# Optimization experiments

Measured on AMD Instinct MI355X. Metric: run time of the kernel, lower is better.

## Reference

```python
import jax, jax.numpy as jnp
import numpy as np


def _maxpool3d(x):
    # 3x3x3 max pool, stride 1, padding 1 (torch pads with -inf for max pool)
    return jax.lax.reduce_window(
        x, -jnp.inf, jax.lax.max,
        window_dimensions=(1, 1, 3, 3, 3),
        window_strides=(1, 1, 1, 1, 1),
        padding=[(0, 0), (0, 0), (1, 1), (1, 1), (1, 1)],
    )


def _soft_erode(x):
    return -_maxpool3d(-x)


def _soft_dilate(x):
    return _maxpool3d(x)


def _soft_open(x):
    return _soft_dilate(_soft_erode(x))


def setup_inputs() -> dict:
    key = jax.random.key(0)
    img = jax.random.uniform(key, (2, 1, 192, 256, 256), dtype=jnp.float32)
    return {"img": img}


def reference(img):
    # NOTE: in the original torch module, `skel` is computed via soft_close +
    # an iterative relu(skel - soft_open(skel)) loop, but the final line
    # `skel = F.relu(img - soft_open(img))` overwrites it entirely, so the
    # loop is dead code and the output depends only on img.
    opened = _soft_open(img)  # dilate(erode(img)), morphological opening
    return jax.nn.relu(img - opened)
```

## Files before the change

kernel.cpp:

```cpp
#include <hip/hip_runtime.h>
#include <math.h>


#define D_ 192
#define H_ 256
#define W_ 256
#define NB 2
#define TH 32
#define TW 64
#define CD 16
#define NCHUNK (D_ / CD)

#define RAW_H (TH + 4)
#define RAW_W (TW + 8)
#define RAW_S 76
#define EB_H  (TH + 2)
#define EB_W  (TW + 8)
#define EB_S  76

#define NRAWF4 (RAW_H * (RAW_W / 4))
#define NBTASK (EB_H * (EB_W / 8))

__device__ __forceinline__ float min3f(float a, float b, float c) {
    return fminf(fminf(a, b), c);
}
__device__ __forceinline__ float max3f(float a, float b, float c) {
    return fmaxf(fmaxf(a, b), c);
}

__global__ __launch_bounds__(256, 3)
void soft_skel_v6(const float* __restrict__ img, float* __restrict__ out) {
    __shared__ __align__(16) float raw[RAW_H][RAW_S];
    __shared__ __align__(16) float ebuf[EB_H][EB_S];

    const int tid  = threadIdx.x;
    const int lane = tid & 63;
    const int w0 = blockIdx.x * TW;
    const int h0 = blockIdx.y * TH;
    const int n  = blockIdx.z / NCHUNK;
    const int ch = blockIdx.z - n * NCHUNK;
    const int z0 = ch * CD;

    const float* vol  = img + (size_t)n * (D_ * H_ * W_);
    float*       ovol = out + (size_t)n * (D_ * H_ * W_);

    const float PINF = INFINITY;

    bool a_slot[3], a_img[3];
    int  a_lds[3], a_off[3];
    #pragma unroll
    for (int k = 0; k < 3; ++k) {
        int idx = tid + 256 * k;
        bool slot = idx < NRAWF4;
        int row = idx / (RAW_W / 4);
        int cg  = idx - row * (RAW_W / 4);
        int gh = h0 - 2 + row;
        int gw = w0 - 4 + 4 * cg;
        a_slot[k] = slot;
        a_img[k]  = slot && (gh >= 0) && (gh < H_) && (gw >= 0) && (gw <= W_ - 4);
        a_off[k]  = gh * W_ + gw;
        a_lds[k]  = slot ? (row * RAW_S + 4 * cg) : 0;
    }

    const int  r0 = tid / 9;
    const int  c0 = (tid - r0 * 9) * 8;
    const bool has1 = tid < (NBTASK - 256);
    const int  t1 = tid + 256;
    const int  r1 = t1 / 9;
    const int  c1 = (t1 - r1 * 9) * 8;

    const int ty = tid >> 3;
    const int cx = tid & 7;
    const int xx = cx * 8;

    float pm0[8], sp0[8], pm1[8], sp1[8];
    float t2A[8], t2B[8], t2C[8];
    float rwA[8], rwB[8], rwC[8];
    #pragma unroll
    for (int j = 0; j < 8; ++j) {
        pm0[j] = sp0[j] = pm1[j] = sp1[j] = PINF;
        t2A[j] = t2B[j] = 0.f;
        rwA[j] = rwB[j] = 0.f;
    }

    auto prefetch = [&](int zz, float4 L[3]) {
        const bool zok = (zz >= 0) && (zz < D_);
        const float* plane = vol + (size_t)zz * (H_ * W_);
        #pragma unroll
        for (int k = 0; k < 3; ++k) {
            float4 v = make_float4(PINF, PINF, PINF, PINF);
            if (zok && a_img[k]) v = *(const float4*)(plane + a_off[k]);
            L[k] = v;
        }
    };

    auto btask = [&](int r, int cb, float pm[8], float sp[8], bool zeok) {
        float4 q00 = *(const float4*)(&raw[r][cb]);
        float4 q01 = *(const float4*)(&raw[r][cb + 4]);
        float4 q10 = *(const float4*)(&raw[r + 1][cb]);
        float4 q11 = *(const float4*)(&raw[r + 1][cb + 4]);
        float4 q20 = *(const float4*)(&raw[r + 2][cb]);
        float4 q21 = *(const float4*)(&raw[r + 2][cb + 4]);
        float v[8];
        v[0] = min3f(q00.x, q10.x, q20.x);
        v[1] = min3f(q00.y, q10.y, q20.y);
        v[2] = min3f(q00.z, q10.z, q20.z);
        v[3] = min3f(q00.w, q10.w, q20.w);
        v[4] = min3f(q01.x, q11.x, q21.x);
        v[5] = min3f(q01.y, q11.y, q21.y);
        v[6] = min3f(q01.z, q11.z, q21.z);
        v[7] = min3f(q01.w, q11.w, q21.w);

        float vL = __shfl_up(v[7], 1);
        float vR = __shfl_down(v[0], 1);
        if (lane == 0) {
            int cl = cb - 1; if (cl < 0) cl = 0;
            vL = min3f(raw[r][cl], raw[r + 1][cl], raw[r + 2][cl]);
        }
        if (lane == 63) {
            int cr = cb + 8; if (cr > RAW_W - 1) cr = RAW_W - 1;
            vR = min3f(raw[r][cr], raw[r + 1][cr], raw[r + 2][cr]);
        }

        float s[8];
        s[0] = min3f(vL, v[0], v[1]);
        #pragma unroll
        for (int j = 1; j < 7; ++j) s[j] = min3f(v[j - 1], v[j], v[j + 1]);
        s[7] = min3f(v[6], v[7], vR);

        const bool rok = zeok && ((unsigned)(h0 - 1 + r) < (unsigned)H_);
        float e[8];
        #pragma unroll
        for (int j = 0; j < 8; ++j) {
            float ev = fminf(pm[j], s[j]);
            bool ok = rok && ((unsigned)(w0 - 4 + cb + j) < (unsigned)W_);
            e[j] = ok ? ev : -PINF;
            pm[j] = fminf(sp[j], s[j]);
            sp[j] = s[j];
        }
        *(float4*)&ebuf[r][cb]     = make_float4(e[0], e[1], e[2], e[3]);
        *(float4*)&ebuf[r][cb + 4] = make_float4(e[4], e[5], e[6], e[7]);
    };

    float4 L[3];
    prefetch(z0 - 2, L);
    const int zzend = z0 + CD + 1;

    for (int zz = z0 - 2; zz <= zzend; ++zz) {
        #pragma unroll
        for (int k = 0; k < 3; ++k)
            if (a_slot[k]) *(float4*)(&raw[0][0] + a_lds[k]) = L[k];
        if (zz < zzend) prefetch(zz + 1, L);
        __syncthreads();

        float4 c0v, c1v;
        const bool zcok = (zz >= 0) && (zz < D_);
        if (zcok) {
            const float* cp = vol + ((size_t)zz * H_ + (h0 + ty)) * W_ + (w0 + xx);
            c0v = *(const float4*)cp;
            c1v = *(const float4*)(cp + 4);
        } else {
            c0v = c1v = make_float4(0.f, 0.f, 0.f, 0.f);
        }

        const int  ze   = zz - 1;
        const bool zeok = (ze >= 0) && (ze < D_);
        btask(r0, c0, pm0, sp0, zeok);
        if (has1) btask(r1, c1, pm1, sp1, zeok);

        rwC[0] = c0v.x; rwC[1] = c0v.y; rwC[2] = c0v.z; rwC[3] = c0v.w;
        rwC[4] = c1v.x; rwC[5] = c1v.y; rwC[6] = c1v.z; rwC[7] = c1v.w;
        __syncthreads();

        {
            const float* p0 = &ebuf[ty][0];
            const float* p1 = &ebuf[ty + 1][0];
            const float* p2 = &ebuf[ty + 2][0];
            float4 q00 = *(const float4*)(p0 + xx + 4);
            float4 q01 = *(const float4*)(p0 + xx + 8);
            float4 q10 = *(const float4*)(p1 + xx + 4);
            float4 q11 = *(const float4*)(p1 + xx + 8);
            float4 q20 = *(const float4*)(p2 + xx + 4);
            float4 q21 = *(const float4*)(p2 + xx + 8);
            float t[8];
            t[0] = max3f(q00.x, q10.x, q20.x);
            t[1] = max3f(q00.y, q10.y, q20.y);
            t[2] = max3f(q00.z, q10.z, q20.z);
            t[3] = max3f(q00.w, q10.w, q20.w);
            t[4] = max3f(q01.x, q11.x, q21.x);
            t[5] = max3f(q01.y, q11.y, q21.y);
            t[6] = max3f(q01.z, q11.z, q21.z);
            t[7] = max3f(q01.w, q11.w, q21.w);

            float tL = __shfl_up(t[7], 1);
            float tR = __shfl_down(t[0], 1);
            if (cx == 0) {
                tL = max3f(p0[xx + 3], p1[xx + 3], p2[xx + 3]);
            }
            if (cx == 7) {
                tR = max3f(p0[xx + 12], p1[xx + 12], p2[xx + 12]);
            }
            t2C[0] = max3f(tL, t[0], t[1]);
            #pragma unroll
            for (int j = 1; j < 7; ++j) t2C[j] = max3f(t[j - 1], t[j], t[j + 1]);
            t2C[7] = max3f(t[6], t[7], tR);
        }

        if (zz >= z0 + 2) {
            const int z = zz - 2;
            float* op = ovol + ((size_t)z * H_ + (h0 + ty)) * W_ + (w0 + xx);
            float o[8];
            #pragma unroll
            for (int j = 0; j < 8; ++j) {
                float opened = max3f(t2A[j], t2B[j], t2C[j]);
                float v = rwA[j] - opened;
                o[j] = v > 0.f ? v : 0.f;
            }
            *(float4*)op       = make_float4(o[0], o[1], o[2], o[3]);
            *(float4*)(op + 4) = make_float4(o[4], o[5], o[6], o[7]);
        }

        #pragma unroll
        for (int j = 0; j < 8; ++j) {
            t2A[j] = t2B[j]; t2B[j] = t2C[j];
            rwA[j] = rwB[j]; rwB[j] = rwC[j];
        }
    }
}

extern "C" void kernel_launch(void* const* d_in, const int* in_sizes, int n_in,
                              void* d_out, int out_size, void* d_ws, size_t ws_size,
                              hipStream_t stream) {
    const float* img = (const float*)d_in[0];
    float* out = (float*)d_out;

    dim3 grid(W_ / TW, H_ / TH, NB * NCHUNK);
    dim3 block(256);
    soft_skel_v6<<<grid, block, 0, stream>>>(img, out);
}
```

Baseline: 195.7 us.

## Double-buffer raw and erosion LDS tiles to drop one barrier per plane

Double-buffers the raw-input and eroded-plane shared-memory tiles so the erosion of plane z and the dilation of plane z-1 run between a single barrier per iteration instead of two. The center voxel values are now read from the previous raw tile in LDS instead of being reloaded from global memory. This adds one more pipeline stage, so each chunk does one extra iteration, and doubles LDS use, which may lower occupancy.

```diff
diff --git a/kernel.cpp b/kernel.cpp
--- a/kernel.cpp
+++ b/kernel.cpp
@@ -29,9 +29,9 @@
 }
 
 __global__ __launch_bounds__(256, 3)
-void soft_skel_v6(const float* __restrict__ img, float* __restrict__ out) {
-    __shared__ __align__(16) float raw[RAW_H][RAW_S];
-    __shared__ __align__(16) float ebuf[EB_H][EB_S];
+void soft_skel_v7(const float* __restrict__ img, float* __restrict__ out) {
+    __shared__ __align__(16) float raw[2][RAW_H][RAW_S];
+    __shared__ __align__(16) float ebuf[2][EB_H][EB_S];
 
     const int tid  = threadIdx.x;
     const int lane = tid & 63;
@@ -75,12 +75,12 @@
 
     float pm0[8], sp0[8], pm1[8], sp1[8];
     float t2A[8], t2B[8], t2C[8];
-    float rwA[8], rwB[8], rwC[8];
+    float rw0[8], rw1[8], rw2[8];
     #pragma unroll
     for (int j = 0; j < 8; ++j) {
         pm0[j] = sp0[j] = pm1[j] = sp1[j] = PINF;
         t2A[j] = t2B[j] = 0.f;
-        rwA[j] = rwB[j] = 0.f;
+        rw0[j] = rw1[j] = 0.f;
     }
 
     auto prefetch = [&](int zz, float4 L[3]) {
@@ -94,13 +94,14 @@
         }
     };
 
-    auto btask = [&](int r, int cb, float pm[8], float sp[8], bool zeok) {
-        float4 q00 = *(const float4*)(&raw[r][cb]);
-        float4 q01 = *(const float4*)(&raw[r][cb + 4]);
-        float4 q10 = *(const float4*)(&raw[r + 1][cb]);
-        float4 q11 = *(const float4*)(&raw[r + 1][cb + 4]);
-        float4 q20 = *(const float4*)(&raw[r + 2][cb]);
-        float4 q21 = *(const float4*)(&raw[r + 2][cb + 4]);
+    auto btask = [&](const float (*rb)[RAW_S], float (*eb)[EB_S],
+                     int r, int cb, float pm[8], float sp[8], bool zeok) {
+        float4 q00 = *(const float4*)(&rb[r][cb]);
+        float4 q01 = *(const float4*)(&rb[r][cb + 4]);
+        float4 q10 = *(const float4*)(&rb[r + 1][cb]);
+        float4 q11 = *(const float4*)(&rb[r + 1][cb + 4]);
+        float4 q20 = *(const float4*)(&rb[r + 2][cb]);
+        float4 q21 = *(const float4*)(&rb[r + 2][cb + 4]);
         float v[8];
         v[0] = min3f(q00.x, q10.x, q20.x);
         v[1] = min3f(q00.y, q10.y, q20.y);
@@ -115,11 +116,11 @@
         float vR = __shfl_down(v[0], 1);
         if (lane == 0) {
             int cl = cb - 1; if (cl < 0) cl = 0;
-            vL = min3f(raw[r][cl], raw[r + 1][cl], raw[r + 2][cl]);
+            vL = min3f(rb[r][cl], rb[r + 1][cl], rb[r + 2][cl]);
         }
         if (lane == 63) {
             int cr = cb + 8; if (cr > RAW_W - 1) cr = RAW_W - 1;
-            vR = min3f(raw[r][cr], raw[r + 1][cr], raw[r + 2][cr]);
+            vR = min3f(rb[r][cr], rb[r + 1][cr], rb[r + 2][cr]);
         }
 
         float s[8];
@@ -138,44 +139,44 @@
             pm[j] = fminf(sp[j], s[j]);
             sp[j] = s[j];
         }
-        *(float4*)&ebuf[r][cb]     = make_float4(e[0], e[1], e[2], e[3]);
-        *(float4*)&ebuf[r][cb + 4] = make_float4(e[4], e[5], e[6], e[7]);
+        *(float4*)&eb[r][cb]     = make_float4(e[0], e[1], e[2], e[3]);
+        *(float4*)&eb[r][cb + 4] = make_float4(e[4], e[5], e[6], e[7]);
     };
 
     float4 L[3];
     prefetch(z0 - 2, L);
-    const int zzend = z0 + CD + 1;
+    const int zzend = z0 + CD + 2;
+    int cur = 0;
 
     for (int zz = z0 - 2; zz <= zzend; ++zz) {
+        float (*rb)[RAW_S]        = raw[cur];
+        const float (*rbp)[RAW_S] = raw[cur ^ 1];
+        float (*eb)[EB_S]         = ebuf[cur];
+        const float (*ebp)[EB_S]  = ebuf[cur ^ 1];
+
         #pragma unroll
         for (int k = 0; k < 3; ++k)
-            if (a_slot[k]) *(float4*)(&raw[0][0] + a_lds[k]) = L[k];
+            if (a_slot[k]) *(float4*)(&rb[0][0] + a_lds[k]) = L[k];
+
+        float4 c0v = *(const float4*)&rbp[ty + 2][xx + 4];
+        float4 c1v = *(const float4*)&rbp[ty + 2][xx + 8];
+
+        __syncthreads();
+
         if (zz < zzend) prefetch(zz + 1, L);
-        __syncthreads();
-
-        float4 c0v, c1v;
-        const bool zcok = (zz >= 0) && (zz < D_);
-        if (zcok) {
-            const float* cp = vol + ((size_t)zz * H_ + (h0 + ty)) * W_ + (w0 + xx);
-            c0v = *(const float4*)cp;
-            c1v = *(const float4*)(cp + 4);
-        } else {
-            c0v = c1v = make_float4(0.f, 0.f, 0.f, 0.f);
-        }
+
+        rw2[0] = c0v.x; rw2[1] = c0v.y; rw2[2] = c0v.z; rw2[3] = c0v.w;
+        rw2[4] = c1v.x; rw2[5] = c1v.y; rw2[6] = c1v.z; rw2[7] = c1v.w;
 
         const int  ze   = zz - 1;
         const bool zeok = (ze >= 0) && (ze < D_);
-        btask(r0, c0, pm0, sp0, zeok);
-        if (has1) btask(r1, c1, pm1, sp1, zeok);
-
-        rwC[0] = c0v.x; rwC[1] = c0v.y; rwC[2] = c0v.z; rwC[3] = c0v.w;
-        rwC[4] = c1v.x; rwC[5] = c1v.y; rwC[6] = c1v.z; rwC[7] = c1v.w;
-        __syncthreads();
+        btask(rb, eb, r0, c0, pm0, sp0, zeok);
+        if (has1) btask(rb, eb, r1, c1, pm1, sp1, zeok);
 
         {
-            const float* p0 = &ebuf[ty][0];
-            const float* p1 = &ebuf[ty + 1][0];
-            const float* p2 = &ebuf[ty + 2][0];
+            const float* p0 = &ebp[ty][0];
+            const float* p1 = &ebp[ty + 1][0];
+            const float* p2 = &ebp[ty + 2][0];
             float4 q00 = *(const float4*)(p0 + xx + 4);
             float4 q01 = *(const float4*)(p0 + xx + 8);
             float4 q10 = *(const float4*)(p1 + xx + 4);
@@ -206,14 +207,14 @@
             t2C[7] = max3f(t[6], t[7], tR);
         }
 
-        if (zz >= z0 + 2) {
-            const int z = zz - 2;
+        if (zz >= z0 + 3) {
+            const int z = zz - 3;
             float* op = ovol + ((size_t)z * H_ + (h0 + ty)) * W_ + (w0 + xx);
             float o[8];
             #pragma unroll
             for (int j = 0; j < 8; ++j) {
                 float opened = max3f(t2A[j], t2B[j], t2C[j]);
-                float v = rwA[j] - opened;
+                float v = rw0[j] - opened;
                 o[j] = v > 0.f ? v : 0.f;
             }
             *(float4*)op       = make_float4(o[0], o[1], o[2], o[3]);
@@ -223,8 +224,9 @@
         #pragma unroll
         for (int j = 0; j < 8; ++j) {
             t2A[j] = t2B[j]; t2B[j] = t2C[j];
-            rwA[j] = rwB[j]; rwB[j] = rwC[j];
-        }
+            rw0[j] = rw1[j]; rw1[j] = rw2[j];
+        }
+        cur ^= 1;
     }
 }
 
@@ -236,5 +238,5 @@
 
     dim3 grid(W_ / TW, H_ / TH, NB * NCHUNK);
     dim3 block(256);
-    soft_skel_v6<<<grid, block, 0, stream>>>(img, out);
-}
+    soft_skel_v7<<<grid, block, 0, stream>>>(img, out);
+}
```

New measurement: 194.0 us. No clear change (-0.9%).
